# Optimization experiments

Measured on AMD Instinct MI355X. Metric: run time of the kernel, lower is better.

The kernel has to match this reference:

```python
import jax, jax.numpy as jnp
import numpy as np

ALPHA = 6.0
BETA = 1.8
D = 256
P = 4096


def setup_inputs() -> dict:
    key = jax.random.key(0)
    k1, k2, k3 = jax.random.split(key, 3)
    pts = jax.random.normal(k1, (1, 16384, 3), dtype=jnp.float32)
    # strict_standard_normal is a shuffled Gaussian quantile grid; a standard
    # normal draw is statistically equivalent for a correctness baseline.
    A = jax.random.normal(k2, (3, D), dtype=jnp.float32) * ALPHA
    B = jax.random.normal(k3, (3, P), dtype=jnp.float32) * BETA
    return {"pts": pts, "A": A, "B": B}


def reference(pts, A, B):
    d = A.shape[-1]
    sqrt_d = jnp.asarray(d, jnp.float32) ** 0.5
    pA = pts @ A            # (b, n, d)
    pB = pts @ B            # (b, n, p)
    eA = jnp.concatenate([jnp.cos(pA), jnp.sin(pA)], axis=-1)  # (b, n, 2d)
    eB = jnp.concatenate([jnp.cos(pB), jnp.sin(pB)], axis=-1)  # (b, n, 2p)
    # linear-attention-style chain: eB @ (eB^T @ eA)
    T = jnp.einsum('bnp,bnd->bpd', eB, eA)   # (b, 2p, 2d)
    G = jnp.einsum('bnp,bpd->bnd', eB, T)    # (b, n, 2d)
    Gc = jax.lax.complex(G[..., :d], G[..., d:]) / jax.lax.complex(eA[..., :d], eA[..., d:])
    Gc = Gc / jnp.linalg.norm(Gc, axis=-1, keepdims=True) * sqrt_d
    return Gc
```

## Files before the change

kernel.cpp:

```cpp
#include <hip/hip_runtime.h>

#define NPTS 16384
#define DH 256
#define PH 4096
#define D2 512
#define LDA 40

typedef _Float16 f16;
typedef _Float16 f16x4 __attribute__((ext_vector_type(4)));
typedef _Float16 f16x8 __attribute__((ext_vector_type(8)));
typedef float f32x4 __attribute__((ext_vector_type(4)));

__device__ f16   g_eAt[D2][NPTS];
__device__ f16   g_Tt[4][D2][2*PH];
__device__ f16   g_Ts[D2][2*PH];
__device__ float g_G[2][NPTS][D2];

__device__ __forceinline__ void gload16(const void* g, void* l) {
    __builtin_amdgcn_global_load_lds((const __attribute__((address_space(1))) void*)g,
                                     (__attribute__((address_space(3))) void*)l, 16, 0, 0);
}

__device__ __forceinline__ void fsincos(float x, float* s, float* c) {
    *s = __sinf(x);
    *c = __cosf(x);
}

__global__ __launch_bounds__(256) void ker_pre(const float* __restrict__ pts,
                                               const float* __restrict__ A) {
    const int dd = blockIdx.x;
    const int t  = threadIdx.x;
    const float a0 = A[dd], a1 = A[DH + dd], a2 = A[2*DH + dd];
    f16* rowc = &g_eAt[dd][t*64];
    f16* rows = &g_eAt[DH + dd][t*64];
    #pragma unroll
    for (int s = 0; s < 8; ++s) {
        const int nb = t*64 + 8*s;
        f16x8 vc, vs;
        #pragma unroll
        for (int i = 0; i < 8; ++i) {
            const float* pr = pts + (size_t)(nb + i)*3;
            float sn, cs_; fsincos(pr[0]*a0 + pr[1]*a1 + pr[2]*a2, &sn, &cs_);
            vc[i] = (f16)cs_; vs[i] = (f16)sn;
        }
        *(f16x8*)(rowc + 8*s) = vc;
        *(f16x8*)(rows + 8*s) = vs;
    }
}

__global__ __launch_bounds__(512) void ker_T(const float* __restrict__ pts,
                                             const float* __restrict__ B) {
    const int q0 = blockIdx.x * 64;
    const int d0 = blockIdx.y * 256;
    const int ks = blockIdx.z;
    const int t  = threadIdx.x;
    const int lane = t & 63, wid = t >> 6;
    const int wm = wid >> 2, wn = wid & 3;

    __shared__ f16 Al[128][LDA];
    __shared__ f16 Bl[256][32];

    f32x4 acc[4][4];
    #pragma unroll
    for (int a = 0; a < 4; ++a)
        #pragma unroll
        for (int bq = 0; bq < 4; ++bq) acc[a][bq] = (f32x4){0.f,0.f,0.f,0.f};

    const int qq  = t >> 3;
    const int nn0 = (t & 7) * 4;
    const float b0 = B[q0+qq], b1 = B[PH+q0+qq], b2 = B[2*PH+q0+qq];
    const size_t bsrc0 = (size_t)(d0 + 32*wid + (lane >> 2))*NPTS + 8*(lane & 3);
    const int mrow = wm*64 + (lane & 15);
    const int ncol = wn*64 + (lane & 15);
    const int kof  = (lane >> 4) * 8;

    for (int c = 0; c < 128; ++c) {
        const int nb = ks*4096 + c*32;
        __syncthreads();
        gload16(&g_eAt[0][0] + bsrc0 + (size_t)nb,                   &Bl[32*wid][0]);
        gload16(&g_eAt[0][0] + bsrc0 + (size_t)16*NPTS + (size_t)nb, &Bl[32*wid + 16][0]);
        {
            const float* pbase = pts + (size_t)(nb + nn0)*3;
            const float4 P0 = *(const float4*)(pbase);
            const float4 P1 = *(const float4*)(pbase + 4);
            const float4 P2 = *(const float4*)(pbase + 8);
            const float px[4] = {P0.x, P0.w, P1.z, P2.y};
            const float py[4] = {P0.y, P1.x, P1.w, P2.z};
            const float pz[4] = {P0.z, P1.y, P2.x, P2.w};
            f16x4 vc, vs;
            #pragma unroll
            for (int u = 0; u < 4; ++u) {
                float sn, cc; fsincos(px[u]*b0 + py[u]*b1 + pz[u]*b2, &sn, &cc);
                vc[u] = (f16)cc; vs[u] = (f16)sn;
            }
            *(f16x4*)&Al[qq][nn0]      = vc;
            *(f16x4*)&Al[64 + qq][nn0] = vs;
        }
        __syncthreads();
        f16x8 af[4], bf[4];
        #pragma unroll
        for (int mf = 0; mf < 4; ++mf) af[mf] = *(const f16x8*)&Al[mrow + mf*16][kof];
        #pragma unroll
        for (int nf = 0; nf < 4; ++nf) bf[nf] = *(const f16x8*)&Bl[ncol + nf*16][kof];
        #pragma unroll
        for (int mf = 0; mf < 4; ++mf)
            #pragma unroll
            for (int nf = 0; nf < 4; ++nf)
                acc[mf][nf] = __builtin_amdgcn_mfma_f32_16x16x32_f16(
                    af[mf], bf[nf], acc[mf][nf], 0, 0, 0);
    }
    #pragma unroll
    for (int mf = 0; mf < 4; ++mf) {
        const int qrow = q0 + mf*16 + (lane >> 4)*4;
        #pragma unroll
        for (int nf = 0; nf < 4; ++nf) {
            const int d = d0 + wn*64 + nf*16 + (lane & 15);
            f16x4 v;
            #pragma unroll
            for (int j = 0; j < 4; ++j) v[j] = (f16)acc[mf][nf][j];
            *(f16x4*)&g_Tt[ks][d][(size_t)wm*PH + qrow] = v;
        }
    }
}

__global__ __launch_bounds__(256) void ker_tsum() {
    const size_t i = ((size_t)blockIdx.x*256 + threadIdx.x) * 8;
    float o[8] = {0,0,0,0,0,0,0,0};
    #pragma unroll
    for (int z = 0; z < 4; ++z) {
        const f16x8 v = *(const f16x8*)(&g_Tt[z][0][0] + i);
        #pragma unroll
        for (int j = 0; j < 8; ++j) o[j] += (float)v[j];
    }
    f16x8 r;
    #pragma unroll
    for (int j = 0; j < 8; ++j) r[j] = (f16)o[j];
    *(f16x8*)(&g_Ts[0][0] + i) = r;
}

__global__ __launch_bounds__(512) void ker_G(const float* __restrict__ pts,
                                             const float* __restrict__ B) {
    const int n0 = blockIdx.x * 128;
    const int d0 = blockIdx.y * 256;
    const int ks = blockIdx.z;
    const int t  = threadIdx.x;
    const int lane = t & 63, wid = t >> 6;
    const int wm = wid >> 2, wn = wid & 3;

    __shared__ f16 Ac[128][LDA], As[128][LDA];
    __shared__ f16 Bc[256][32],  Bs[256][32];

    f32x4 acc[4][4];
    #pragma unroll
    for (int a = 0; a < 4; ++a)
        #pragma unroll
        for (int bq = 0; bq < 4; ++bq) acc[a][bq] = (f32x4){0.f,0.f,0.f,0.f};

    const int nn  = t >> 2;
    const int qq0 = (t & 3) * 8;
    const float px = pts[(size_t)(n0+nn)*3];
    const float py = pts[(size_t)(n0+nn)*3 + 1];
    const float pz = pts[(size_t)(n0+nn)*3 + 2];
    const size_t bsrc0 = (size_t)(d0 + 32*wid + (lane >> 2))*(2*PH) + 8*(lane & 3);
    const int mrow = wm*64 + (lane & 15);
    const int ncol = wn*64 + (lane & 15);
    const int kof  = (lane >> 4) * 8;

    for (int c = 0; c < 64; ++c) {
        const int qk = ks*2048 + c*32;
        __syncthreads();
        gload16(&g_Ts[0][0] + bsrc0 + (size_t)qk,                            &Bc[32*wid][0]);
        gload16(&g_Ts[0][0] + bsrc0 + (size_t)16*(2*PH) + (size_t)qk,        &Bc[32*wid + 16][0]);
        gload16(&g_Ts[0][0] + bsrc0 + (size_t)PH + (size_t)qk,               &Bs[32*wid][0]);
        gload16(&g_Ts[0][0] + bsrc0 + (size_t)(16*(2*PH) + PH) + (size_t)qk, &Bs[32*wid + 16][0]);
        {
            const int qg = qk + qq0;
            const float4 bx0 = *(const float4*)&B[qg];
            const float4 bx1 = *(const float4*)&B[qg + 4];
            const float4 by0 = *(const float4*)&B[PH + qg];
            const float4 by1 = *(const float4*)&B[PH + qg + 4];
            const float4 bz0 = *(const float4*)&B[2*PH + qg];
            const float4 bz1 = *(const float4*)&B[2*PH + qg + 4];
            const float bx[8] = {bx0.x,bx0.y,bx0.z,bx0.w, bx1.x,bx1.y,bx1.z,bx1.w};
            const float by[8] = {by0.x,by0.y,by0.z,by0.w, by1.x,by1.y,by1.z,by1.w};
            const float bz[8] = {bz0.x,bz0.y,bz0.z,bz0.w, bz1.x,bz1.y,bz1.z,bz1.w};
            f16x8 vc, vs;
            #pragma unroll
            for (int u = 0; u < 8; ++u) {
                float sn, cc; fsincos(px*bx[u] + py*by[u] + pz*bz[u], &sn, &cc);
                vc[u] = (f16)cc; vs[u] = (f16)sn;
            }
            *(f16x8*)&Ac[nn][qq0] = vc;
            *(f16x8*)&As[nn][qq0] = vs;
        }
        __syncthreads();
        f16x8 a1[4], a2[4], b1[4], b2[4];
        #pragma unroll
        for (int mf = 0; mf < 4; ++mf) {
            a1[mf] = *(const f16x8*)&Ac[mrow + mf*16][kof];
            a2[mf] = *(const f16x8*)&As[mrow + mf*16][kof];
        }
        #pragma unroll
        for (int nf = 0; nf < 4; ++nf) {
            b1[nf] = *(const f16x8*)&Bc[ncol + nf*16][kof];
            b2[nf] = *(const f16x8*)&Bs[ncol + nf*16][kof];
        }
        #pragma unroll
        for (int mf = 0; mf < 4; ++mf)
            #pragma unroll
            for (int nf = 0; nf < 4; ++nf) {
                acc[mf][nf] = __builtin_amdgcn_mfma_f32_16x16x32_f16(
                    a1[mf], b1[nf], acc[mf][nf], 0, 0, 0);
                acc[mf][nf] = __builtin_amdgcn_mfma_f32_16x16x32_f16(
                    a2[mf], b2[nf], acc[mf][nf], 0, 0, 0);
            }
    }
    #pragma unroll
    for (int mf = 0; mf < 4; ++mf) {
        const int nbase = n0 + wm*64 + mf*16 + (lane >> 4)*4;
        #pragma unroll
        for (int nf = 0; nf < 4; ++nf) {
            const int d = d0 + wn*64 + nf*16 + (lane & 15);
            #pragma unroll
            for (int j = 0; j < 4; ++j)
                g_G[ks][nbase + j][d] = acc[mf][nf][j];
        }
    }
}

__global__ __launch_bounds__(256) void ker_fin(const float* __restrict__ pts,
                                               const float* __restrict__ A,
                                               float* __restrict__ out) {
    const int n = blockIdx.x;
    const int k = threadIdx.x;
    const float p0 = pts[(size_t)n*3], p1 = pts[(size_t)n*3+1], p2 = pts[(size_t)n*3+2];
    const float alp = p0*A[k] + p1*A[DH + k] + p2*A[2*DH + k];
    float sa, ca; fsincos(alp, &sa, &ca);
    const float Gr = g_G[0][n][k]      + g_G[1][n][k];
    const float Gi = g_G[0][n][DH + k] + g_G[1][n][DH + k];
    const float Re = Gr*ca + Gi*sa;
    float nr = Gr*Gr + Gi*Gi;
    #pragma unroll
    for (int off = 32; off > 0; off >>= 1) nr += __shfl_down(nr, off, 64);
    __shared__ float wsum[4];
    if ((k & 63) == 0) wsum[k >> 6] = nr;
    __syncthreads();
    const float total = wsum[0] + wsum[1] + wsum[2] + wsum[3];
    const float scale = 16.0f * rsqrtf(total);
    out[(size_t)n*DH + k] = Re * scale;
}

extern "C" void kernel_launch(void* const* d_in, const int* in_sizes, int n_in,
                              void* d_out, int out_size, void* d_ws, size_t ws_size,
                              hipStream_t stream) {
    const float* pts = (const float*)d_in[0];
    const float* A   = (const float*)d_in[1];
    const float* B   = (const float*)d_in[2];
    float* out = (float*)d_out;
    (void)d_ws; (void)ws_size; (void)out_size;

    ker_pre <<<256, 256, 0, stream>>>(pts, A);
    ker_T   <<<dim3(64, 2, 4), 512, 0, stream>>>(pts, B);
    ker_tsum<<<2048, 256, 0, stream>>>();
    ker_G   <<<dim3(128, 2, 2), 512, 0, stream>>>(pts, B);
    ker_fin <<<16384, 256, 0, stream>>>(pts, A, out);
}
```

Baseline: 390.1 us.

## Double T-kernel K tile to 64 and XOR-swizzle eA layout for conflict-free LDS

```diff
diff --git a/kernel.cpp b/kernel.cpp
--- a/kernel.cpp
+++ b/kernel.cpp
@@ -5,13 +5,14 @@
 #define PH 4096
 #define D2 512
 #define LDA 40
+#define LDT 72
 
 typedef _Float16 f16;
 typedef _Float16 f16x4 __attribute__((ext_vector_type(4)));
 typedef _Float16 f16x8 __attribute__((ext_vector_type(8)));
 typedef float f32x4 __attribute__((ext_vector_type(4)));
 
-__device__ f16   g_eAt[D2][NPTS];
+__device__ f16   g_eAtS[(size_t)D2 * NPTS];
 __device__ f16   g_Tt[4][D2][2*PH];
 __device__ f16   g_Ts[D2][2*PH];
 __device__ float g_G[2][NPTS][D2];
@@ -22,8 +23,7 @@
 }
 
 __device__ __forceinline__ void fsincos(float x, float* s, float* c) {
-    *s = __sinf(x);
-    *c = __cosf(x);
+    *s = __sinf(x); *c = __cosf(x);
 }
 
 __global__ __launch_bounds__(256) void ker_pre(const float* __restrict__ pts,
@@ -31,11 +31,12 @@
     const int dd = blockIdx.x;
     const int t  = threadIdx.x;
     const float a0 = A[dd], a1 = A[DH + dd], a2 = A[2*DH + dd];
-    f16* rowc = &g_eAt[dd][t*64];
-    f16* rows = &g_eAt[DH + dd][t*64];
+    f16* rowc = &g_eAtS[(size_t)dd*NPTS + t*64];
+    f16* rows = &g_eAtS[(size_t)(DH + dd)*NPTS + t*64];
+    const int sx = dd & 7;
     #pragma unroll
     for (int s = 0; s < 8; ++s) {
-        const int nb = t*64 + 8*s;
+        const int nb = t*64 + 8*(s ^ sx);
         f16x8 vc, vs;
         #pragma unroll
         for (int i = 0; i < 8; ++i) {
@@ -56,9 +57,10 @@
     const int t  = threadIdx.x;
     const int lane = t & 63, wid = t >> 6;
     const int wm = wid >> 2, wn = wid & 3;
-
-    __shared__ f16 Al[128][LDA];
-    __shared__ f16 Bl[256][32];
+    const int l7 = lane & 7;
+
+    __shared__ f16 Al[128][LDT];
+    __shared__ f16 Bl[256][64];
 
     f32x4 acc[4][4];
     #pragma unroll
@@ -67,47 +69,56 @@
         for (int bq = 0; bq < 4; ++bq) acc[a][bq] = (f32x4){0.f,0.f,0.f,0.f};
 
     const int qq  = t >> 3;
-    const int nn0 = (t & 7) * 4;
+    const int nn0 = (t & 7) * 8;
     const float b0 = B[q0+qq], b1 = B[PH+q0+qq], b2 = B[2*PH+q0+qq];
-    const size_t bsrc0 = (size_t)(d0 + 32*wid + (lane >> 2))*NPTS + 8*(lane & 3);
+    const size_t bsrc0 = (size_t)(d0 + 32*wid + (lane >> 3))*NPTS + 8*l7;
     const int mrow = wm*64 + (lane & 15);
     const int ncol = wn*64 + (lane & 15);
-    const int kof  = (lane >> 4) * 8;
-
-    for (int c = 0; c < 128; ++c) {
-        const int nb = ks*4096 + c*32;
-        __syncthreads();
-        gload16(&g_eAt[0][0] + bsrc0 + (size_t)nb,                   &Bl[32*wid][0]);
-        gload16(&g_eAt[0][0] + bsrc0 + (size_t)16*NPTS + (size_t)nb, &Bl[32*wid + 16][0]);
+
+    for (int c = 0; c < 64; ++c) {
+        const int nb = ks*4096 + c*64;
+        __syncthreads();
+        #pragma unroll
+        for (int i = 0; i < 4; ++i)
+            gload16(&g_eAtS[0] + bsrc0 + (size_t)(8*i)*NPTS + (size_t)nb,
+                    &Bl[32*wid + 8*i][0]);
         {
-            const float* pbase = pts + (size_t)(nb + nn0)*3;
-            const float4 P0 = *(const float4*)(pbase);
-            const float4 P1 = *(const float4*)(pbase + 4);
-            const float4 P2 = *(const float4*)(pbase + 8);
-            const float px[4] = {P0.x, P0.w, P1.z, P2.y};
-            const float py[4] = {P0.y, P1.x, P1.w, P2.z};
-            const float pz[4] = {P0.z, P1.y, P2.x, P2.w};
-            f16x4 vc, vs;
-            #pragma unroll
-            for (int u = 0; u < 4; ++u) {
-                float sn, cc; fsincos(px[u]*b0 + py[u]*b1 + pz[u]*b2, &sn, &cc);
+            const float* pb = pts + (size_t)(nb + nn0)*3;
+            const float4 F0 = *(const float4*)(pb);
+            const float4 F1 = *(const float4*)(pb + 4);
+            const float4 F2 = *(const float4*)(pb + 8);
+            const float4 F3 = *(const float4*)(pb + 12);
+            const float4 F4 = *(const float4*)(pb + 16);
+            const float4 F5 = *(const float4*)(pb + 20);
+            const float xx[8] = {F0.x, F0.w, F1.z, F2.y, F3.x, F3.w, F4.z, F5.y};
+            const float yy[8] = {F0.y, F1.x, F1.w, F2.z, F3.y, F4.x, F4.w, F5.z};
+            const float zz[8] = {F0.z, F1.y, F2.x, F2.w, F3.z, F4.y, F5.x, F5.w};
+            f16x8 vc, vs;
+            #pragma unroll
+            for (int u = 0; u < 8; ++u) {
+                float sn, cc; fsincos(xx[u]*b0 + yy[u]*b1 + zz[u]*b2, &sn, &cc);
                 vc[u] = (f16)cc; vs[u] = (f16)sn;
             }
-            *(f16x4*)&Al[qq][nn0]      = vc;
-            *(f16x4*)&Al[64 + qq][nn0] = vs;
-        }
-        __syncthreads();
-        f16x8 af[4], bf[4];
-        #pragma unroll
-        for (int mf = 0; mf < 4; ++mf) af[mf] = *(const f16x8*)&Al[mrow + mf*16][kof];
-        #pragma unroll
-        for (int nf = 0; nf < 4; ++nf) bf[nf] = *(const f16x8*)&Bl[ncol + nf*16][kof];
-        #pragma unroll
-        for (int mf = 0; mf < 4; ++mf)
+            *(f16x8*)&Al[qq][nn0]      = vc;
+            *(f16x8*)&Al[64 + qq][nn0] = vs;
+        }
+        __syncthreads();
+        #pragma unroll
+        for (int kk = 0; kk < 2; ++kk) {
+            f16x8 af[4], bf[4];
+            #pragma unroll
+            for (int mf = 0; mf < 4; ++mf)
+                af[mf] = *(const f16x8*)&Al[mrow + mf*16][32*kk + (lane >> 4)*8];
             #pragma unroll
             for (int nf = 0; nf < 4; ++nf)
-                acc[mf][nf] = __builtin_amdgcn_mfma_f32_16x16x32_f16(
-                    af[mf], bf[nf], acc[mf][nf], 0, 0, 0);
+                bf[nf] = *(const f16x8*)&Bl[ncol + nf*16][(((lane >> 4) + 4*kk) ^ l7)*8];
+            #pragma unroll
+            for (int mf = 0; mf < 4; ++mf)
+                #pragma unroll
+                for (int nf = 0; nf < 4; ++nf)
+                    acc[mf][nf] = __builtin_amdgcn_mfma_f32_16x16x32_f16(
+                        af[mf], bf[nf], acc[mf][nf], 0, 0, 0);
+        }
     }
     #pragma unroll
     for (int mf = 0; mf < 4; ++mf) {
```

Result: faster. 369.0 us (-5.4%).
